# Performance work log

Measured on AMD Instinct MI355X. Metric: run time of the kernel, lower is better.

Reference implementation:

```python
import jax, jax.numpy as jnp
import numpy as np
from jax import lax

B, C, H, W = 16, 256, 64, 64  # inplanes=256, planes=2*inplanes=512


def ste_sign(x):
    # forward: sign(x); backward: clipped straight-through (|x|<=1)
    c = jnp.clip(x, -1.0, 1.0)
    return c + lax.stop_gradient(jnp.sign(x) - c)


def conv_ada(x, w, ka, kw):
    # 1-bit activations scaled by learnable scalar ka
    a_b = ste_sign(x) * ka
    # 1-bit weights with per-out-channel XNOR-style scale * learnable kw
    alpha = jnp.mean(jnp.abs(w), axis=(1, 2, 3), keepdims=True) * kw  # [O,1,1,1]
    w_b = ste_sign(w) * alpha
    return lax.conv_general_dilated(a_b, w_b, window_strides=(1, 1),
                                    padding=((1, 1), (1, 1)),
                                    dimension_numbers=('NCHW', 'OIHW', 'NCHW'))


def prelu(x, slope):
    s = slope.reshape(1, -1, 1, 1)
    return jnp.where(x >= 0, x, s * x)


def pixel_unshuffle2(x):
    b, c, h, w = x.shape
    x = x.reshape(b, c, h // 2, 2, w // 2, 2)
    x = x.transpose(0, 1, 3, 5, 2, 4)  # (b, c, r1, r2, h2, w2)
    return x.reshape(b, c * 4, h // 2, w // 2)


def setup_inputs() -> dict:
    key = jax.random.key(0)
    ks = jax.random.split(key, 8)
    inp = {
        'x': jax.random.normal(ks[0], (B, C, H, W), dtype=jnp.float32),
        'conv1_w': jax.random.normal(ks[1], (C, C, 3, 3), dtype=jnp.float32) * 0.05,
        'conv2_w': jax.random.normal(ks[2], (C // 2, C, 3, 3), dtype=jnp.float32) * 0.05,
        'bias1_': jnp.zeros((1, C, 1, 1), jnp.float32),
        'bias1': jnp.zeros((1, C, 1, 1), jnp.float32),
        'bias2': jnp.zeros((1, C, 1, 1), jnp.float32),
        'bias2_': jnp.zeros((1, C, 1, 1), jnp.float32),
        'bias3': jnp.zeros((1, C // 2, 1, 1), jnp.float32),
        'bias4': jnp.zeros((1, C // 2, 1, 1), jnp.float32),
        'ka1': jnp.asarray(1.0, jnp.float32),
        'kw1': jnp.asarray(0.2, jnp.float32),
        'ka2': jnp.asarray(1.0, jnp.float32),
        'kw2': jnp.asarray(0.2, jnp.float32),
        'prelu1_w': jnp.full((C,), 0.25, jnp.float32),
        'prelu2_w': jnp.full((C // 2,), 0.25, jnp.float32),
    }
    return inp


def reference(x, conv1_w, conv2_w, bias1_, bias1, bias2, bias2_, bias3, bias4,
              ka1, kw1, ka2, kw2, prelu1_w, prelu2_w):
    out = x + bias1_                      # move1_
    out = conv_ada(out, conv1_w, ka1, kw1)  # conv1
    xres = out + x                        # residual add
    # NOTE: in the original forward, move1/prelu1/move2 output is overwritten
    # (dead branch); kept here for faithfulness but it does not affect output.
    _dead = prelu(out + bias1, prelu1_w) + bias2
    out = xres + bias2_                   # move2_
    out = conv_ada(out, conv2_w, ka2, kw2)  # conv2 -> C//2 channels
    shortcut = xres[:, :xres.shape[1] // 2, :, :]
    out = out + shortcut
    out = out + bias3                     # move3
    out = prelu(out, prelu2_w)            # prelu2
    out = out + bias4                     # move4
    out = pixel_unshuffle2(out)           # -> [B, 2*C, H/2, W/2]
    return out
```

## Files before the change

### kernel.cpp

```cpp
#include <hip/hip_runtime.h>
#include <hip/hip_bf16.h>
#include <stdint.h>

#define B_   16
#define C_   256
#define H_   64
#define W_   64
#define PH   66
#define PW   66
#define K1   2304
#define NO1  256
#define NO2  128

typedef signed char i8;
typedef int   int32x4 __attribute__((ext_vector_type(4)));

__device__ __forceinline__ void gl_lds16(const void* src, void* dst) {
    __builtin_amdgcn_global_load_lds(
        (const __attribute__((address_space(1))) unsigned int*)src,
        (__attribute__((address_space(3))) unsigned int*)dst, 16, 0, 0);
}

__device__ __forceinline__ i8 sign_i8(float v) {
    return (v > 0.f) ? (i8)1 : ((v < 0.f) ? (i8)(-1) : (i8)0);
}

__global__ void prep_s1(const float* __restrict__ x, const float* __restrict__ bias1_,
                        i8* __restrict__ s1, i8* __restrict__ s2) {
    __shared__ i8 tile[64][272];
    int b = blockIdx.x >> 6;
    int h = blockIdx.x & 63;
    int t = threadIdx.x;
    int w  = t & 63;
    int cq = t >> 6;
    for (int i = 0; i < 64; ++i) {
        int c = cq * 64 + i;
        float v = x[((size_t)(b * C_ + c) * H_ + h) * W_ + w] + bias1_[c];
        tile[w][c] = sign_i8(v);
    }
    __syncthreads();
    for (int i = 0; i < 4; ++i) {
        int idx = i * 256 + t;
        int w2  = idx >> 4;
        int cb  = (idx & 15) * 16;
        int4 v = *(const int4*)&tile[w2][cb];
        *(int4*)(s1 + ((size_t)(b * PH + h + 1) * PW + (w2 + 1)) * C_ + cb) = v;
    }
    int4 z = make_int4(0, 0, 0, 0);
    if (t < 64) {
        int which = t >> 4;
        int c16   = t & 15;
        i8* base  = (which < 2) ? s1 : s2;
        int col   = (which & 1) ? 65 : 0;
        *(int4*)(base + ((size_t)(b * PH + h + 1) * PW + col) * C_ + c16 * 16) = z;
    }
    if (h == 0 || h == 63) {
        int prow = (h == 0) ? 0 : 65;
        for (int i = 0; i < 9; ++i) {
            int idx = i * 256 + t;
            if (idx < 2112) {
                i8* base = (idx < 1056) ? s1 : s2;
                int k    = (idx < 1056) ? idx : idx - 1056;
                *(int4*)(base + ((size_t)(b * PH + prow) * PW) * C_ + k * 16) = z;
            }
        }
    }
}

__global__ void prep_w(const float* __restrict__ w1, const float* __restrict__ w2,
                       const float* __restrict__ ka1, const float* __restrict__ kw1,
                       const float* __restrict__ ka2, const float* __restrict__ kw2,
                       i8* __restrict__ Bt1, i8* __restrict__ Bt2,
                       float* __restrict__ scale1, float* __restrict__ scale2) {
    int o = blockIdx.x;
    const float* w; i8* Bt; float* scale; float kk;
    if (o < NO1) { w = w1 + (size_t)o * K1;         Bt = Bt1 + (size_t)o * K1;         scale = scale1 + o;         kk = ka1[0] * kw1[0]; }
    else         { int oo = o - NO1;
                   w = w2 + (size_t)oo * K1;        Bt = Bt2 + (size_t)oo * K1;        scale = scale2 + oo;        kk = ka2[0] * kw2[0]; }
    int t = threadIdx.x;
    float s = 0.f;
    for (int e = t; e < K1; e += 256) {
        float v = w[e];
        s += fabsf(v);
        int c = e / 9, tap = e % 9;
        Bt[tap * 256 + c] = sign_i8(v);
    }
    for (int off = 32; off; off >>= 1) s += __shfl_down(s, off);
    __shared__ float red[4];
    if ((t & 63) == 0) red[t >> 6] = s;
    __syncthreads();
    if (t == 0) {
        float tot = red[0] + red[1] + red[2] + red[3];
        *scale = kk * tot * (1.0f / 2304.0f);
    }
}

template<int EPI>
__device__ __forceinline__ void conv_body(
               char* Alds,
               const i8* __restrict__ Sin, const i8* __restrict__ Bt,
               const float* __restrict__ scale,
               const float* __restrict__ xaux,
               const float* __restrict__ biasA,
               const float* __restrict__ bias4,
               const float* __restrict__ slope,
               i8*   __restrict__ s2out,
               float* __restrict__ xres_out,
               float* __restrict__ dout)
{
    int t  = threadIdx.x;

    int wg    = blockIdx.x;
    int chunk = gridDim.x >> 3;
    int logical = (wg & 7) * chunk + (wg >> 3);
    int nb, mb;
    if (EPI == 1) { nb = logical & 1; mb = logical >> 1; }
    else          { nb = 0;           mb = logical; }
    int b  = mb >> 4;
    int h0 = (mb & 15) * 4;

    int l  = t & 63;
    int wv = t >> 6;
    int wr = wv >> 1;
    int wc = wv & 1;
    int q  = l >> 4;

    for (int i = 0; i < 13; ++i) {
        int idx = i * 512 + t;
        if (idx < 6336) {
            int r6   = idx / 1056;
            int rem  = idx - r6 * 1056;
            int w66  = rem >> 4;
            int slot = rem & 15;
            int pix  = r6 * 66 + w66;
            const i8* ga = Sin + ((size_t)(b * PH + h0 + r6) * PW + w66) * 256
                               + ((slot ^ (pix & 7)) << 4);
            gl_lds16(ga, Alds + idx * 16);
        }
    }
    asm volatile("s_waitcnt vmcnt(0)" ::: "memory");
    __builtin_amdgcn_s_barrier();

    int pixbase[4];
#pragma unroll
    for (int mi = 0; mi < 4; ++mi) {
        int m = wr * 64 + mi * 16 + (l & 15);
        pixbase[mi] = (m >> 6) * 66 + (m & 63);
    }
    const i8* bptr[4];
#pragma unroll
    for (int ni = 0; ni < 4; ++ni) {
        int n = nb * 128 + wc * 64 + ni * 16 + (l & 15);
        bptr[ni] = Bt + (size_t)n * K1 + q * 16;
    }

    int32x4 acc[4][4];
#pragma unroll
    for (int mi = 0; mi < 4; ++mi)
#pragma unroll
        for (int ni = 0; ni < 4; ++ni) acc[mi][ni] = (int32x4){0, 0, 0, 0};

    auto loadB = [&](int ks, int32x4 (&dst)[8]) {
#pragma unroll
        for (int ni = 0; ni < 4; ++ni) {
            dst[ni * 2 + 0] = *(const int32x4*)(bptr[ni] + ks * 128);
            dst[ni * 2 + 1] = *(const int32x4*)(bptr[ni] + ks * 128 + 64);
        }
    };

    auto step = [&](int ks, const int32x4 (&bfr)[8]) {
        int tap  = ks >> 1;
        int toff = (tap / 3) * 66 + (tap % 3);
        int c8   = (ks & 1) << 7;
#pragma unroll
        for (int kk = 0; kk < 2; ++kk) {
            int qk = kk * 4 + q;
            int32x4 af[4];
#pragma unroll
            for (int mi = 0; mi < 4; ++mi) {
                int pixm = pixbase[mi] + toff;
                af[mi] = *(const int32x4*)(Alds + pixm * 256 + c8 + ((qk ^ (pixm & 7)) << 4));
            }
#pragma unroll
            for (int mi = 0; mi < 4; ++mi)
#pragma unroll
                for (int ni = 0; ni < 4; ++ni)
                    acc[mi][ni] = __builtin_amdgcn_mfma_i32_16x16x64_i8(af[mi], bfr[ni * 2 + kk], acc[mi][ni], 0, 0, 0);
        }
    };

    int32x4 bA[8], bB[8];
    loadB(0, bA);
#pragma unroll
    for (int ks2 = 0; ks2 < 9; ++ks2) {
        loadB(2 * ks2 + 1, bB);
        step(2 * ks2, bA);
        if (ks2 < 8) loadB(2 * ks2 + 2, bA);
        step(2 * ks2 + 1, bB);
    }

    int co = l & 15;
    int ro = l >> 4;
#pragma unroll
    for (int mi = 0; mi < 4; ++mi) {
#pragma unroll
        for (int ni = 0; ni < 4; ++ni) {
            int n_loc = wc * 64 + ni * 16 + co;
            int o = nb * 128 + n_loc;
            float sc = scale[o];
#pragma unroll
            for (int j = 0; j < 4; ++j) {
                int m_loc = wr * 64 + mi * 16 + ro * 4 + j;
                int h = h0 + (m_loc >> 6);
                int w = m_loc & 63;
                float v = (float)acc[mi][ni][j] * sc;
                if (EPI == 1) {
                    float xv = xaux[((size_t)(b * C_ + o) * H_ + h) * W_ + w];
                    float xr = v + xv;
                    float sv = xr + biasA[o];
                    s2out[((size_t)(b * PH + h + 1) * PW + (w + 1)) * C_ + o] = sign_i8(sv);
                    if (o < NO2)
                        xres_out[(((size_t)b * H_ + h) * W_ + w) * NO2 + o] = xr;
                } else {
                    float xr = xaux[(((size_t)b * H_ + h) * W_ + w) * NO2 + o];
                    float vv = v + xr + biasA[o];
                    vv = (vv >= 0.f) ? vv : vv * slope[o];
                    vv += bias4[o];
                    int p = h & 1, qq = w & 1;
                    dout[(((size_t)b * 512 + (o * 4 + p * 2 + qq)) * 32 + (h >> 1)) * 32 + (w >> 1)] = vv;
                }
            }
        }
    }
}

__global__ __launch_bounds__(512) void conv_g1(
    const i8* Sin, const i8* Bt, const float* scale, const float* xaux,
    const float* biasA, const float* bias4, const float* slope,
    i8* s2out, float* xres_out, float* dout) {
    extern __shared__ char lds[];
    conv_body<1>(lds, Sin, Bt, scale, xaux, biasA, bias4, slope, s2out, xres_out, dout);
}
__global__ __launch_bounds__(512) void conv_g2(
    const i8* Sin, const i8* Bt, const float* scale, const float* xaux,
    const float* biasA, const float* bias4, const float* slope,
    i8* s2out, float* xres_out, float* dout) {
    extern __shared__ char lds[];
    conv_body<2>(lds, Sin, Bt, scale, xaux, biasA, bias4, slope, s2out, xres_out, dout);
}

static const size_t SZ_S   = (size_t)B_ * PH * PW * C_;
static const size_t OFF_S1 = 0;
static const size_t OFF_S2 = OFF_S1 + SZ_S;
static const size_t OFF_B1 = OFF_S2 + SZ_S;
static const size_t OFF_B2 = OFF_B1 + (size_t)NO1 * K1;
static const size_t OFF_C1 = OFF_B2 + (size_t)NO2 * K1;
static const size_t OFF_C2 = OFF_C1 + 1024;
static const size_t OFF_XR = OFF_C2 + 512;

static const int LDS_BYTES = 101376;

extern "C" void kernel_launch(void* const* d_in, const int* in_sizes, int n_in,
                              void* d_out, int out_size, void* d_ws, size_t ws_size,
                              hipStream_t stream) {
    (void)in_sizes; (void)n_in; (void)out_size; (void)ws_size;
    const float* x      = (const float*)d_in[0];
    const float* w1     = (const float*)d_in[1];
    const float* w2     = (const float*)d_in[2];
    const float* bias1_ = (const float*)d_in[3];
    const float* bias2_ = (const float*)d_in[6];
    const float* bias3  = (const float*)d_in[7];
    const float* bias4  = (const float*)d_in[8];
    const float* ka1    = (const float*)d_in[9];
    const float* kw1    = (const float*)d_in[10];
    const float* ka2    = (const float*)d_in[11];
    const float* kw2    = (const float*)d_in[12];
    const float* slope2 = (const float*)d_in[14];

    char* ws = (char*)d_ws;
    i8*    s1   = (i8*)(ws + OFF_S1);
    i8*    s2   = (i8*)(ws + OFF_S2);
    i8*    Bt1  = (i8*)(ws + OFF_B1);
    i8*    Bt2  = (i8*)(ws + OFF_B2);
    float* sc1  = (float*)(ws + OFF_C1);
    float* sc2  = (float*)(ws + OFF_C2);
    float* xres = (float*)(ws + OFF_XR);
    float* out  = (float*)d_out;

    hipLaunchKernelGGL(prep_s1, dim3(B_ * H_), dim3(256), 0, stream, x, bias1_, s1, s2);
    hipLaunchKernelGGL(prep_w, dim3(NO1 + NO2), dim3(256), 0, stream,
                       w1, w2, ka1, kw1, ka2, kw2, Bt1, Bt2, sc1, sc2);
    hipLaunchKernelGGL(conv_g1, dim3(512), dim3(512), LDS_BYTES, stream,
                       s1, Bt1, sc1, x, bias2_, nullptr, nullptr, s2, xres, nullptr);
    hipLaunchKernelGGL(conv_g2, dim3(256), dim3(512), LDS_BYTES, stream,
                       s2, Bt2, sc2, xres, bias3, bias4, slope2, nullptr, nullptr, out);
}
```

Baseline: 312.8 us.

## Stage conv weights through triple-buffered LDS and vectorize sign prep loads

```diff
diff --git a/kernel.cpp b/kernel.cpp
--- a/kernel.cpp
+++ b/kernel.cpp
@@ -31,12 +31,16 @@
     int b = blockIdx.x >> 6;
     int h = blockIdx.x & 63;
     int t = threadIdx.x;
-    int w  = t & 63;
-    int cq = t >> 6;
-    for (int i = 0; i < 64; ++i) {
-        int c = cq * 64 + i;
-        float v = x[((size_t)(b * C_ + c) * H_ + h) * W_ + w] + bias1_[c];
-        tile[w][c] = sign_i8(v);
+    int w4 = (t & 15) * 4;
+    int cg = t >> 4;
+    for (int i = 0; i < 16; ++i) {
+        int c = i * 16 + cg;
+        float4 v = *(const float4*)&x[((size_t)(b * C_ + c) * H_ + h) * W_ + w4];
+        float bb = bias1_[c];
+        tile[w4 + 0][c] = sign_i8(v.x + bb);
+        tile[w4 + 1][c] = sign_i8(v.y + bb);
+        tile[w4 + 2][c] = sign_i8(v.z + bb);
+        tile[w4 + 3][c] = sign_i8(v.w + bb);
     }
     __syncthreads();
     for (int i = 0; i < 4; ++i) {
@@ -108,6 +112,10 @@
                float* __restrict__ xres_out,
                float* __restrict__ dout)
 {
+    char* Bs0 = Alds + 101376;
+    char* Bs1 = Bs0 + 16384;
+    char* Bs2 = Bs1 + 16384;
+
     int t  = threadIdx.x;
 
     int wg    = blockIdx.x;
@@ -125,6 +133,21 @@
     int wc = wv & 1;
     int q  = l >> 4;
 
+    int br0  = t >> 3;
+    int bsrc = ((t & 7) * 16) ^ (((t >> 3) & 7) << 4);
+    int blin = (t & 7) * 16;
+
+    auto stageB_half = [&](int ks, char* Bs, int half) {
+        int tap = ks >> 1;
+        int c0  = (ks & 1) * 128;
+        int r   = br0 + half * 64;
+        int n   = nb * 128 + r;
+        const i8* gb = Bt + (size_t)n * K1 + tap * 256 + c0 + bsrc;
+        gl_lds16(gb, Bs + r * 128 + blin);
+    };
+
+    stageB_half(0, Bs0, 0); stageB_half(0, Bs0, 1);
+    stageB_half(1, Bs1, 0); stageB_half(1, Bs1, 1);
     for (int i = 0; i < 13; ++i) {
         int idx = i * 512 + t;
         if (idx < 6336) {
@@ -147,12 +170,13 @@
         int m = wr * 64 + mi * 16 + (l & 15);
         pixbase[mi] = (m >> 6) * 66 + (m & 63);
     }
-    const i8* bptr[4];
-#pragma unroll
-    for (int ni = 0; ni < 4; ++ni) {
-        int n = nb * 128 + wc * 64 + ni * 16 + (l & 15);
-        bptr[ni] = Bt + (size_t)n * K1 + q * 16;
-    }
+    int rx = (l & 7) << 4;
+    int bfbase[4];
+#pragma unroll
+    for (int ni = 0; ni < 4; ++ni)
+        bfbase[ni] = (wc * 64 + ni * 16 + (l & 15)) * 128;
+    int bfoff0 = (q * 16) ^ rx;
+    int bfoff1 = (64 + q * 16) ^ rx;
 
     int32x4 acc[4][4];
 #pragma unroll
@@ -160,43 +184,58 @@
 #pragma unroll
         for (int ni = 0; ni < 4; ++ni) acc[mi][ni] = (int32x4){0, 0, 0, 0};
 
-    auto loadB = [&](int ks, int32x4 (&dst)[8]) {
-#pragma unroll
-        for (int ni = 0; ni < 4; ++ni) {
-            dst[ni * 2 + 0] = *(const int32x4*)(bptr[ni] + ks * 128);
-            dst[ni * 2 + 1] = *(const int32x4*)(bptr[ni] + ks * 128 + 64);
-        }
-    };
-
-    auto step = [&](int ks, const int32x4 (&bfr)[8]) {
+    char* pr = Bs0; char* pn = Bs1; char* ps = Bs2;
+
+    for (int ks = 0; ks < 18; ++ks) {
         int tap  = ks >> 1;
         int toff = (tap / 3) * 66 + (tap % 3);
         int c8   = (ks & 1) << 7;
-#pragma unroll
-        for (int kk = 0; kk < 2; ++kk) {
-            int qk = kk * 4 + q;
-            int32x4 af[4];
+
+        {
+            int32x4 af[4], bf[4];
 #pragma unroll
             for (int mi = 0; mi < 4; ++mi) {
                 int pixm = pixbase[mi] + toff;
-                af[mi] = *(const int32x4*)(Alds + pixm * 256 + c8 + ((qk ^ (pixm & 7)) << 4));
+                af[mi] = *(const int32x4*)(Alds + pixm * 256 + c8 + ((q ^ (pixm & 7)) << 4));
             }
 #pragma unroll
+            for (int ni = 0; ni < 4; ++ni)
+                bf[ni] = *(const int32x4*)(pr + bfbase[ni] + bfoff0);
+            if (ks < 16) stageB_half(ks + 2, ps, 0);
+            __builtin_amdgcn_s_barrier();
+            __builtin_amdgcn_s_setprio(1);
+#pragma unroll
             for (int mi = 0; mi < 4; ++mi)
 #pragma unroll
                 for (int ni = 0; ni < 4; ++ni)
-                    acc[mi][ni] = __builtin_amdgcn_mfma_i32_16x16x64_i8(af[mi], bfr[ni * 2 + kk], acc[mi][ni], 0, 0, 0);
-        }
-    };
-
-    int32x4 bA[8], bB[8];
-    loadB(0, bA);
-#pragma unroll
-    for (int ks2 = 0; ks2 < 9; ++ks2) {
-        loadB(2 * ks2 + 1, bB);
-        step(2 * ks2, bA);
-        if (ks2 < 8) loadB(2 * ks2 + 2, bA);
-        step(2 * ks2 + 1, bB);
+                    acc[mi][ni] = __builtin_amdgcn_mfma_i32_16x16x64_i8(af[mi], bf[ni], acc[mi][ni], 0, 0, 0);
+            __builtin_amdgcn_s_setprio(0);
+            __builtin_amdgcn_s_barrier();
+        }
+        {
+            int32x4 af[4], bf[4];
+#pragma unroll
+            for (int mi = 0; mi < 4; ++mi) {
+                int pixm = pixbase[mi] + toff;
+                af[mi] = *(const int32x4*)(Alds + pixm * 256 + c8 + (((4 + q) ^ (pixm & 7)) << 4));
+            }
+#pragma unroll
+            for (int ni = 0; ni < 4; ++ni)
+                bf[ni] = *(const int32x4*)(pr + bfbase[ni] + bfoff1);
+            if (ks < 16) stageB_half(ks + 2, ps, 1);
+            __builtin_amdgcn_s_barrier();
+            __builtin_amdgcn_s_setprio(1);
+#pragma unroll
+            for (int mi = 0; mi < 4; ++mi)
+#pragma unroll
+                for (int ni = 0; ni < 4; ++ni)
+                    acc[mi][ni] = __builtin_amdgcn_mfma_i32_16x16x64_i8(af[mi], bf[ni], acc[mi][ni], 0, 0, 0);
+            __builtin_amdgcn_s_setprio(0);
+            if (ks < 16)       asm volatile("s_waitcnt vmcnt(2)" ::: "memory");
+            else if (ks == 16) asm volatile("s_waitcnt vmcnt(0)" ::: "memory");
+            if (ks < 17) __builtin_amdgcn_s_barrier();
+        }
+        char* tmp = pr; pr = pn; pn = ps; ps = tmp;
     }
 
     int co = l & 15;
@@ -258,7 +297,7 @@
 static const size_t OFF_C2 = OFF_C1 + 1024;
 static const size_t OFF_XR = OFF_C2 + 512;
 
-static const int LDS_BYTES = 101376;
+static const int LDS_BYTES = 101376 + 3 * 16384;
 
 extern "C" void kernel_launch(void* const* d_in, const int* in_sizes, int n_in,
                               void* d_out, int out_size, void* d_ws, size_t ws_size,
```

After: 270.9 us. 1.15x faster.
